# Kernel optimization log

Measured on AMD Instinct MI355X. Metric: run time of the kernel, lower is better.

The kernel has to match this reference:

```python
import jax, jax.numpy as jnp
import numpy as np

KH = KW = 3
SH = SW = 1
PH = PW = 1
EPS = 1e-6


def _unfold(x, kh, kw, sh, sw, ph, pw):
    """Replicates torch.nn.functional.unfold: returns [B, C*kh*kw, L]."""
    x = jnp.pad(x, ((0, 0), (0, 0), (ph, ph), (pw, pw)))
    B, C, H, W = x.shape
    Ho = (H - kh) // sh + 1
    Wo = (W - kw) // sw + 1
    # channel-major, then (kh, kw) ordering, matching F.unfold
    cols = jnp.stack(
        [x[:, :, i:i + (Ho - 1) * sh + 1:sh, j:j + (Wo - 1) * sw + 1:sw]
         for i in range(kh) for j in range(kw)],
        axis=2,
    )  # [B, C, kh*kw, Ho, Wo]
    return cols.reshape(B, C * kh * kw, Ho * Wo), Ho, Wo


def setup_inputs() -> dict:
    key = jax.random.key(0)
    k1, k2, k3 = jax.random.split(key, 3)
    x = jax.random.normal(k1, (4, 32, 32, 32), dtype=jnp.float32)
    positions = jax.random.uniform(k2, (32, 32, 3, 3, 5), dtype=jnp.float32,
                                   minval=-1.0, maxval=1.0)
    values = jax.random.normal(k3, (32, 32, 3, 3, 5), dtype=jnp.float32) * 0.01
    return {"x": x, "positions": positions, "values": values}


def _piecewise_conv(x, positions, values):
    O, C, kh, kw, P = positions.shape
    patches, Ho, Wo = _unfold(x, KH, KW, SH, SW, PH, PW)  # [B, T, L]
    T = C * kh * kw
    B = x.shape[0]
    L = Ho * Wo

    pos = positions.reshape(O, T, P)
    val = values.reshape(O, T, P)
    # forward sorts each (out_ch, input) table by position
    order = jnp.argsort(pos, axis=-1)
    pos = jnp.take_along_axis(pos, order, axis=-1)
    val = jnp.take_along_axis(val, order, axis=-1)

    xv = patches.transpose(0, 2, 1)          # [B, L, T]
    xb = xv[:, None, :, :]                   # [B, 1, L, T]

    # interval index: last j with pos[j] <= x (== count(pos <= x) - 1)
    cnt = jnp.sum(pos[None, :, None, :, :] <= xb[..., None], axis=-1)  # [B,O,L,T]
    idx = jnp.clip(cnt - 1, 0, P - 2)

    def gather(tab, ind):
        # tab: [O, T, P], ind: [B, O, L, T] -> [B, O, L, T]
        ind2 = ind.transpose(1, 3, 0, 2).reshape(O, T, B * L)
        out = jnp.take_along_axis(tab, ind2, axis=-1)
        return out.reshape(O, T, B, L).transpose(2, 0, 3, 1)

    pos_j = gather(pos, idx)
    pos_j1 = gather(pos, idx + 1)
    val_j = gather(val, idx)
    val_j1 = gather(val, idx + 1)

    t = jnp.clip((xb - pos_j) / (pos_j1 - pos_j + EPS), 0.0, 1.0)
    interp = val_j + t * (val_j1 - val_j)
    res = jnp.where(pos_j == pos_j1, val_j, interp)

    first = pos[None, :, None, :, 0]
    last = pos[None, :, None, :, P - 1]
    v0 = val[None, :, None, :, 0]
    vl = val[None, :, None, :, P - 1]
    res = jnp.where(xb <= first, v0, jnp.where(xb >= last, vl, res))

    out = res.sum(axis=-1)                   # [B, O, L]
    return out.reshape(B, O, Ho, Wo)


def reference(x, positions, values):
    return _piecewise_conv(x, positions, values)
```

## Files before the change

### kernel.cpp

```cpp
#include <hip/hip_runtime.h>

#define B_  4
#define O_  32
#define C_  32
#define H_  32
#define W_  32
#define P_  5
#define T_  288
#define PIX (H_ * W_)
#define EPSF 1e-6f

#define NCH 2
#define CG  (C_ / NCH)
#define NO  2
#define OG  (O_ / NO)

#define ENT (NO * NCH * 9)
#define TABF (ENT * 16)

#define XROW 34
#define XSTR 35
#define XS_PER_CH (XROW * XSTR)
#define NSTAGE (NCH * XROW * XROW)

__global__ __launch_bounds__(256, 4) void pw_conv(
    const float* __restrict__ x, const float* __restrict__ pos,
    const float* __restrict__ val, float* __restrict__ part)
{
    __shared__ float xs[NCH * XS_PER_CH];
    __shared__ float ts[TABF];

    const int cg = blockIdx.x;
    const int og = blockIdx.y;
    const int b  = blockIdx.z;
    const int tid = threadIdx.x;
    const int c0 = cg * NCH;
    const int o0 = og * NO;

    const float* xb = x + (b * C_ + c0) * PIX;
#define STAGE_ONE(IDX)                                                     \
    {                                                                      \
        int _idx = (IDX);                                                  \
        int _ch  = _idx / (XROW * XROW);                                   \
        int _rem = _idx - _ch * (XROW * XROW);                             \
        int _r   = _rem / XROW;                                            \
        int _col = _rem - _r * XROW;                                       \
        int _gr = _r - 1, _gc = _col - 1;                                  \
        float _v = 0.f;                                                    \
        if ((unsigned)_gr < (unsigned)H_ && (unsigned)_gc < (unsigned)W_)  \
            _v = xb[_ch * PIX + _gr * W_ + _gc];                           \
        xs[_ch * XS_PER_CH + _r * XSTR + _col] = _v;                       \
    }
#pragma unroll
    for (int k = 0; k < NSTAGE / 256; ++k)
        STAGE_ONE(tid + k * 256);
    if (tid < NSTAGE - (NSTAGE / 256) * 256)
        STAGE_ONE(tid + (NSTAGE / 256) * 256);
#undef STAGE_ONE

    if (tid < ENT) {
        const int oo = tid / (NCH * 9);
        const int rem = tid - oo * (NCH * 9);
        const int id = (o0 + oo) * T_ + c0 * 9 + rem;

        const float* pp = pos + id * P_;
        const float* vv = val + id * P_;
        float p0 = pp[0], p1 = pp[1], p2 = pp[2], p3 = pp[3], p4 = pp[4];
        float v0 = vv[0], v1 = vv[1], v2 = vv[2], v3 = vv[3], v4 = vv[4];

#define CSWAP(a, bb, va, vb)                        \
        {                                           \
            float _pa = fminf(a, bb), _pb = fmaxf(a, bb); \
            bool _sw = (a > bb);                    \
            float _va = _sw ? vb : va;              \
            float _vb = _sw ? va : vb;              \
            a = _pa; bb = _pb; va = _va; vb = _vb;  \
        }
        CSWAP(p0, p1, v0, v1);
        CSWAP(p3, p4, v3, v4);
        CSWAP(p2, p4, v2, v4);
        CSWAP(p2, p3, v2, v3);
        CSWAP(p1, p4, v1, v4);
        CSWAP(p0, p3, v0, v3);
        CSWAP(p0, p2, v0, v2);
        CSWAP(p1, p3, v1, v3);
        CSWAP(p1, p2, v1, v2);
#undef CSWAP

        float inv0 = 1.0f / (p1 - p0 + EPSF);
        float inv1 = 1.0f / (p2 - p1 + EPSF);
        float inv2 = 1.0f / (p3 - p2 + EPSF);
        float inv3 = 1.0f / (p4 - p3 + EPSF);

        float* e = ts + tid * 16;
        e[0]  = inv0;        e[1]  = inv1;        e[2]  = inv2;        e[3]  = inv3;
        e[4]  = -p0 * inv0;  e[5]  = -p1 * inv1;  e[6]  = -p2 * inv2;  e[7]  = -p3 * inv3;
        e[8]  = v1 - v0;     e[9]  = v2 - v1;     e[10] = v3 - v2;     e[11] = v4 - v3;
        e[12] = v0;          e[13] = 0.f;         e[14] = 0.f;         e[15] = 0.f;
    }
    __syncthreads();

    const int r  = tid >> 3;
    const int c4 = (tid & 7) * 4;

    float sv0[NO];
#pragma unroll
    for (int oo = 0; oo < NO; ++oo) {
        float s = 0.f;
#pragma unroll
        for (int e = 0; e < NCH * 9; ++e)
            s += ts[(oo * NCH * 9 + e) * 16 + 12];
        sv0[oo] = s;
    }

    float acc[NO][4];
#pragma unroll
    for (int oo = 0; oo < NO; ++oo)
#pragma unroll
        for (int k = 0; k < 4; ++k)
            acc[oo][k] = sv0[oo];

#pragma unroll
    for (int ch = 0; ch < NCH; ++ch) {
        float xr[3][6];
#pragma unroll
        for (int i = 0; i < 3; ++i)
#pragma unroll
            for (int j = 0; j < 6; ++j)
                xr[i][j] = xs[ch * XS_PER_CH + (r + i) * XSTR + c4 + j];

#pragma unroll
        for (int oo = 0; oo < NO; ++oo) {
            const float4* e4 = (const float4*)(ts + (oo * NCH + ch) * 9 * 16);
#pragma unroll
            for (int ij = 0; ij < 9; ++ij) {
                const int i = ij / 3, j = ij % 3;
                const float4 qi = e4[ij * 4 + 0];
                const float4 qf = e4[ij * 4 + 1];
                const float4 qd = e4[ij * 4 + 2];

#define EVAL(ACC, XV)                                                        \
                {                                                            \
                    float _xv = (XV);                                        \
                    float _t;                                                \
                    _t = __builtin_amdgcn_fmed3f(fmaf(_xv, qi.x, qf.x), 0.f, 1.f); \
                    ACC = fmaf(_t, qd.x, ACC);                               \
                    _t = __builtin_amdgcn_fmed3f(fmaf(_xv, qi.y, qf.y), 0.f, 1.f); \
                    ACC = fmaf(_t, qd.y, ACC);                               \
                    _t = __builtin_amdgcn_fmed3f(fmaf(_xv, qi.z, qf.z), 0.f, 1.f); \
                    ACC = fmaf(_t, qd.z, ACC);                               \
                    _t = __builtin_amdgcn_fmed3f(fmaf(_xv, qi.w, qf.w), 0.f, 1.f); \
                    ACC = fmaf(_t, qd.w, ACC);                               \
                }
                EVAL(acc[oo][0], xr[i][j + 0]);
                EVAL(acc[oo][1], xr[i][j + 1]);
                EVAL(acc[oo][2], xr[i][j + 2]);
                EVAL(acc[oo][3], xr[i][j + 3]);
#undef EVAL
            }
        }
    }

#pragma unroll
    for (int oo = 0; oo < NO; ++oo) {
        float4 res;
        res.x = acc[oo][0]; res.y = acc[oo][1];
        res.z = acc[oo][2]; res.w = acc[oo][3];
        float4* pp = (float4*)(part + ((size_t)(cg * B_ + b) * O_ + o0 + oo) * PIX);
        pp[tid] = res;
    }
}

__global__ __launch_bounds__(256) void reduce16(
    const float* __restrict__ part, float* __restrict__ out)
{
    int j = blockIdx.x * 256 + threadIdx.x;
    const float4* p4 = (const float4*)part;
    float4 s; s.x = 0.f; s.y = 0.f; s.z = 0.f; s.w = 0.f;
#pragma unroll
    for (int cg = 0; cg < CG; ++cg) {
        float4 p = p4[cg * (B_ * O_ * PIX / 4) + j];
        s.x += p.x; s.y += p.y; s.z += p.z; s.w += p.w;
    }
    ((float4*)out)[j] = s;
}

extern "C" void kernel_launch(void* const* d_in, const int* in_sizes, int n_in,
                              void* d_out, int out_size, void* d_ws, size_t ws_size,
                              hipStream_t stream)
{
    const float* x   = (const float*)d_in[0];
    const float* pos = (const float*)d_in[1];
    const float* val = (const float*)d_in[2];

    float* part = (float*)d_ws;

    dim3 grid(CG, OG, B_);
    pw_conv<<<grid, 256, 0, stream>>>(x, pos, val, part);

    int n4 = B_ * O_ * PIX / 4;
    reduce16<<<n4 / 256, 256, 0, stream>>>(part, (float*)d_out);
}
```

Measured before the change: 78.47 us.

## Remap threads to one output channel and two rows, vectorize LDS reads

Each thread now handles a single output channel across two adjacent output rows instead of two output channels on one row. This lets the 4x6 input window be shared across two rows, and it is read with float4/float2 LDS loads enabled by padding the row stride to 36. Per thread, LDS input reads drop and table reads are halved. The risks are extra register pressure and possible LDS bank conflicts from the aligned stride.

```diff
diff --git a/kernel.cpp b/kernel.cpp
--- a/kernel.cpp
+++ b/kernel.cpp
@@ -19,7 +19,7 @@
 #define TABF (ENT * 16)
 
 #define XROW 34
-#define XSTR 35
+#define XSTR 36
 #define XS_PER_CH (XROW * XSTR)
 #define NSTAGE (NCH * XROW * XROW)
 
@@ -100,74 +100,74 @@
     }
     __syncthreads();
 
-    const int r  = tid >> 3;
-    const int c4 = (tid & 7) * 4;
-
-    float sv0[NO];
-#pragma unroll
-    for (int oo = 0; oo < NO; ++oo) {
-        float s = 0.f;
-#pragma unroll
-        for (int e = 0; e < NCH * 9; ++e)
-            s += ts[(oo * NCH * 9 + e) * 16 + 12];
-        sv0[oo] = s;
-    }
-
-    float acc[NO][4];
-#pragma unroll
-    for (int oo = 0; oo < NO; ++oo)
+    const int oo = tid >> 7;
+    const int lt = tid & 127;
+    const int r0 = (lt >> 3) * 2;
+    const int c4 = (lt & 7) * 4;
+
+    float sv0 = 0.f;
+#pragma unroll
+    for (int e = 0; e < NCH * 9; ++e)
+        sv0 += ts[(oo * NCH * 9 + e) * 16 + 12];
+
+    float acc[2][4];
+#pragma unroll
+    for (int dr = 0; dr < 2; ++dr)
 #pragma unroll
         for (int k = 0; k < 4; ++k)
-            acc[oo][k] = sv0[oo];
+            acc[dr][k] = sv0;
 
 #pragma unroll
     for (int ch = 0; ch < NCH; ++ch) {
-        float xr[3][6];
-#pragma unroll
-        for (int i = 0; i < 3; ++i)
-#pragma unroll
-            for (int j = 0; j < 6; ++j)
-                xr[i][j] = xs[ch * XS_PER_CH + (r + i) * XSTR + c4 + j];
-
-#pragma unroll
-        for (int oo = 0; oo < NO; ++oo) {
-            const float4* e4 = (const float4*)(ts + (oo * NCH + ch) * 9 * 16);
-#pragma unroll
-            for (int ij = 0; ij < 9; ++ij) {
-                const int i = ij / 3, j = ij % 3;
-                const float4 qi = e4[ij * 4 + 0];
-                const float4 qf = e4[ij * 4 + 1];
-                const float4 qd = e4[ij * 4 + 2];
+        float xw[4][6];
+#pragma unroll
+        for (int i = 0; i < 4; ++i) {
+            const float* base = &xs[ch * XS_PER_CH + (r0 + i) * XSTR + c4];
+            float4 q  = *(const float4*)(base);
+            float2 q2 = *(const float2*)(base + 4);
+            xw[i][0] = q.x;  xw[i][1] = q.y;  xw[i][2] = q.z;  xw[i][3] = q.w;
+            xw[i][4] = q2.x; xw[i][5] = q2.y;
+        }
+
+        const float4* e4 = (const float4*)(ts + (oo * NCH + ch) * 9 * 16);
+#pragma unroll
+        for (int ij = 0; ij < 9; ++ij) {
+            const int i = ij / 3, j = ij % 3;
+            const float4 qi = e4[ij * 4 + 0];
+            const float4 qf = e4[ij * 4 + 1];
+            const float4 qd = e4[ij * 4 + 2];
 
 #define EVAL(ACC, XV)                                                        \
-                {                                                            \
-                    float _xv = (XV);                                        \
-                    float _t;                                                \
-                    _t = __builtin_amdgcn_fmed3f(fmaf(_xv, qi.x, qf.x), 0.f, 1.f); \
-                    ACC = fmaf(_t, qd.x, ACC);                               \
-                    _t = __builtin_amdgcn_fmed3f(fmaf(_xv, qi.y, qf.y), 0.f, 1.f); \
-                    ACC = fmaf(_t, qd.y, ACC);                               \
-                    _t = __builtin_amdgcn_fmed3f(fmaf(_xv, qi.z, qf.z), 0.f, 1.f); \
-                    ACC = fmaf(_t, qd.z, ACC);                               \
-                    _t = __builtin_amdgcn_fmed3f(fmaf(_xv, qi.w, qf.w), 0.f, 1.f); \
-                    ACC = fmaf(_t, qd.w, ACC);                               \
-                }
-                EVAL(acc[oo][0], xr[i][j + 0]);
-                EVAL(acc[oo][1], xr[i][j + 1]);
-                EVAL(acc[oo][2], xr[i][j + 2]);
-                EVAL(acc[oo][3], xr[i][j + 3]);
+            {                                                                \
+                float _xv = (XV);                                            \
+                float _t;                                                    \
+                _t = __builtin_amdgcn_fmed3f(fmaf(_xv, qi.x, qf.x), 0.f, 1.f); \
+                ACC = fmaf(_t, qd.x, ACC);                                   \
+                _t = __builtin_amdgcn_fmed3f(fmaf(_xv, qi.y, qf.y), 0.f, 1.f); \
+                ACC = fmaf(_t, qd.y, ACC);                                   \
+                _t = __builtin_amdgcn_fmed3f(fmaf(_xv, qi.z, qf.z), 0.f, 1.f); \
+                ACC = fmaf(_t, qd.z, ACC);                                   \
+                _t = __builtin_amdgcn_fmed3f(fmaf(_xv, qi.w, qf.w), 0.f, 1.f); \
+                ACC = fmaf(_t, qd.w, ACC);                                   \
+            }
+#pragma unroll
+            for (int dr = 0; dr < 2; ++dr) {
+                EVAL(acc[dr][0], xw[dr + i][j + 0]);
+                EVAL(acc[dr][1], xw[dr + i][j + 1]);
+                EVAL(acc[dr][2], xw[dr + i][j + 2]);
+                EVAL(acc[dr][3], xw[dr + i][j + 3]);
+            }
 #undef EVAL
-            }
         }
     }
 
-#pragma unroll
-    for (int oo = 0; oo < NO; ++oo) {
+    float* op = part + ((size_t)(cg * B_ + b) * O_ + o0 + oo) * PIX;
+#pragma unroll
+    for (int dr = 0; dr < 2; ++dr) {
         float4 res;
-        res.x = acc[oo][0]; res.y = acc[oo][1];
-        res.z = acc[oo][2]; res.w = acc[oo][3];
-        float4* pp = (float4*)(part + ((size_t)(cg * B_ + b) * O_ + o0 + oo) * PIX);
-        pp[tid] = res;
+        res.x = acc[dr][0]; res.y = acc[dr][1];
+        res.z = acc[dr][2]; res.w = acc[dr][3];
+        *(float4*)(op + (r0 + dr) * W_ + c4) = res;
     }
 }
 
```

New measurement: 75.43 us. -3.9%, faster.
